# Kernel tuning notes

Hardware: AMD Instinct MI355X
Metric: run time of the kernel (lower is better)

## Reference

```python
import jax, jax.numpy as jnp
import numpy as np

N_WAY, N_SHOT = 10, 15
N_QUERY, D = 8192, 1024
C_REG = 0.1
MAX_ITER = 15


def setup_inputs() -> dict:
    key = jax.random.key(0)
    k1, k2 = jax.random.split(key)
    n_sup = N_WAY * N_SHOT
    feat = jax.random.normal(k1, (n_sup + N_QUERY, D), dtype=jnp.float32) * 0.1
    label_support = jnp.arange(N_WAY, dtype=jnp.int32)
    label_query = jax.random.randint(k2, (N_QUERY,), 0, N_WAY, dtype=jnp.int32)
    scale = jnp.ones((1,), dtype=jnp.float32)
    return {"feat": feat, "label_support": label_support,
            "label_query": label_query, "scale": scale}


def _qp_solve(Q, p, h, A):
    """min 0.5 z'Qz + p'z  s.t.  z <= h,  A z = 0.
    Infeasible-start primal-dual interior-point method, MAX_ITER fixed iterations
    (mirrors qpth's QPFunction(maxIter=15) iterative batched-solve structure)."""
    n = Q.shape[0]
    m = A.shape[0]
    dtype = Q.dtype
    z = h - 1.0                      # slack s = h - z = 1 > 0
    s = jnp.ones((n,), dtype)
    lam = jnp.ones((n,), dtype)
    nu = jnp.zeros((m,), dtype)
    sigma = jnp.asarray(0.1, dtype)  # centering parameter

    def step(carry, _):
        z, s, lam, nu = carry
        mu = jnp.dot(s, lam) / n
        rd = Q @ z + p + lam + A.T @ nu      # dual residual
        rp = A @ z                           # primal (equality) residual, b = 0
        rc = s * lam - sigma * mu            # complementarity residual
        r1 = -rd + rc / s
        H = Q + jnp.diag(lam / s)
        L = jnp.linalg.cholesky(H)
        solveH = lambda r: jax.scipy.linalg.cho_solve((L, True), r)
        Hinv_AT = solveH(A.T)                # (n, m)
        Hinv_r1 = solveH(r1)                 # (n,)
        S = A @ Hinv_AT                      # (m, m) Schur complement
        dnu = jnp.linalg.solve(S, A @ Hinv_r1 + rp)
        dz = Hinv_r1 - Hinv_AT @ dnu
        ds = -dz
        dlam = (lam * dz - rc) / s

        def max_step(v, dv):                 # largest alpha keeping v + alpha*dv > 0
            ratios = jnp.where(dv < 0, -v / jnp.where(dv < 0, dv, -1.0), jnp.inf)
            return jnp.min(ratios)

        alpha = jnp.minimum(1.0, 0.99 * jnp.minimum(max_step(s, ds), max_step(lam, dlam)))
        return (z + alpha * dz, s + alpha * ds, lam + alpha * dlam, nu + alpha * dnu), None

    (z, s, lam, nu), _ = jax.lax.scan(step, (z, s, lam, nu), None, length=MAX_ITER)
    return z


def reference(feat, label_support, label_query, scale):
    n_way, n_shot = N_WAY, N_SHOT
    n_sup = n_way * n_shot
    support = feat[:n_sup]                       # (n_sup, d)
    query = feat[n_sup:]                         # (n_q, d)
    sup_labels = jnp.repeat(label_support, n_shot)   # label[0].repeat_interleave(n_shot)

    K = support @ support.T                      # Gram matrix (n_sup, n_sup)
    n = n_sup * n_way
    eye_w = jnp.eye(n_way, dtype=K.dtype)
    # batched_kronecker(K, I_way): index (i*n_way + a)
    Q = jnp.einsum('ij,ab->iajb', K, eye_w).reshape(n, n) + 10.0 * jnp.eye(n, dtype=K.dtype)
    y_onehot = jax.nn.one_hot(sup_labels, n_way, dtype=K.dtype).reshape(n)
    p = -y_onehot                                # e
    h = C_REG * y_onehot                         # box: z <= C_reg * Y (C = I)
    # A = kron(I_{n_sup}, ones(1, n_way))
    A = jnp.einsum('ij,a->ija', jnp.eye(n_sup, dtype=K.dtype),
                   jnp.ones((n_way,), K.dtype)).reshape(n_sup, n)

    qp_sol = _qp_solve(Q, p, h, A).reshape(n_sup, n_way)

    compat = support @ query.T                   # (n_sup, n_q)
    # logits[q, w] = sum_s compat[s, q] * qp_sol[s, w]
    logits = scale[0] * jnp.einsum('sq,sw->qw', compat, qp_sol)
    log_prb = jax.nn.log_softmax(logits, axis=1)     # (n_q, n_way)
    y_q = jax.nn.one_hot(label_query, n_way, dtype=log_prb.dtype)
    loss = -(y_q * log_prb).sum(axis=1).mean()
    return (log_prb, loss)
```

## Files before the change

kernel.cpp:

```cpp
#include <hip/hip_runtime.h>


#define NW    10
#define NSH   15
#define NSUP  150
#define NQ    8192
#define DIM   1024
#define NVAR  1500
#define NP    152
#define NTT   19
#define NACT  (NTT*NTT)
#define TPB   384
#define SIGMA 0.1f
#define PSTR  68

#define OFF_K     0
#define OFF_Z     22800
#define OFF_S     24300
#define OFF_LAM   25800
#define OFF_R1    27300
#define OFF_DZ    28800
#define OFF_DLAM  30300
#define OFF_G     31800
#define OFF_NU0   33300
#define OFF_NU1   33452
#define OFF_DNU   33604
#define OFF_DOTS  33756
#define OFF_MU    33786
#define OFF_SLOT  33788
#define OFF_LP    33792
#define OFF_WT    35840
#define OFF_SMAT  46080
#define OFF_X     69184
#define XSZ       (NP*NP)

__device__ __forceinline__ void bgj_core(float (&H)[8][8], const int t, const int tr, const int tc,
                                         float (*rowbuf)[PSTR], float (*colbuf)[NTT][PSTR],
                                         float (*wbuf)[PSTR]) {
  const int lane = t & 63;
  const int pr = lane >> 3, pc = lane & 7;
  const int r8 = t & 7;
  const int wj2 = t >> 3;
  const int jb = wj2 >> 1;
  const int jh4 = (wj2 & 1) << 2;
  const bool wact = (t < 8*NTT*2);
  const bool act = (t < NACT);
  for (int kb = 0; kb < NTT; ++kb) {
    const int cur = kb & 1, nxt = cur ^ 1;
    float p = rowbuf[kb][lane];
#pragma unroll
    for (int pp = 0; pp < 8; ++pp) {
      const float pv   = __shfl(p, pp*9, 64);
      const float d    = 1.0f / pv;
      const float rowv = __shfl(p, pp*8 + pc, 64);
      const float colv = __shfl(p, pr*8 + pp, 64);
      const float nr   = rowv * d;
      float v = fmaf(-colv, nr, p);
      if (pr == pp) v = nr;
      if (pc == pp) v = -colv * d;
      if (pr == pp && pc == pp) v = d;
      p = v;
    }
    float pv8[8];
#pragma unroll
    for (int q = 0; q < 8; ++q) pv8[q] = __shfl(p, r8*8 + q, 64);
    if (wact) {
      float w0, w1, w2, w3;
      if (jb == kb) {
        w0 = jh4 ? pv8[4] : pv8[0]; w1 = jh4 ? pv8[5] : pv8[1];
        w2 = jh4 ? pv8[6] : pv8[2]; w3 = jh4 ? pv8[7] : pv8[3];
      } else {
        w0 = w1 = w2 = w3 = 0.0f;
#pragma unroll
        for (int q = 0; q < 8; ++q) {
          const float4 x = *(const float4*)(&rowbuf[jb][q*8 + jh4]);
          w0 = fmaf(pv8[q], x.x, w0); w1 = fmaf(pv8[q], x.y, w1);
          w2 = fmaf(pv8[q], x.z, w2); w3 = fmaf(pv8[q], x.w, w3);
        }
      }
      *(float4*)(&wbuf[jb][r8*8 + jh4]) = make_float4(w0, w1, w2, w3);
    }
    __syncthreads();
    if (act) {
      if (tr == kb) {
        const float4* wsrc = (const float4*)(&wbuf[tc][0]);
#pragma unroll
        for (int r = 0; r < 8; ++r) {
          const float4 x = wsrc[2*r], y = wsrc[2*r+1];
          H[r][0]=x.x; H[r][1]=x.y; H[r][2]=x.z; H[r][3]=x.w;
          H[r][4]=y.x; H[r][5]=y.y; H[r][6]=y.z; H[r][7]=y.w;
        }
      } else {
        float C[8][8];
        const float4* cs = (const float4*)(&colbuf[cur][tr][0]);
#pragma unroll
        for (int r = 0; r < 8; ++r) {
          const float4 x = cs[2*r], y = cs[2*r+1];
          C[r][0]=x.x; C[r][1]=x.y; C[r][2]=x.z; C[r][3]=x.w;
          C[r][4]=y.x; C[r][5]=y.y; C[r][6]=y.z; C[r][7]=y.w;
        }
        if (tc == kb) {
#pragma unroll
          for (int r = 0; r < 8; ++r)
#pragma unroll
            for (int c = 0; c < 8; ++c) H[r][c] = 0.0f;
        }
        const float4* wsrc = (const float4*)(&wbuf[tc][0]);
#pragma unroll
        for (int q = 0; q < 8; ++q) {
          const float4 x = wsrc[2*q], y = wsrc[2*q+1];
          const float w0=x.x,w1=x.y,w2=x.z,w3=x.w,w4=y.x,w5=y.y,w6=y.z,w7=y.w;
#pragma unroll
          for (int r = 0; r < 8; ++r) {
            const float cq = C[r][q];
            H[r][0]=fmaf(-cq,w0,H[r][0]); H[r][1]=fmaf(-cq,w1,H[r][1]);
            H[r][2]=fmaf(-cq,w2,H[r][2]); H[r][3]=fmaf(-cq,w3,H[r][3]);
            H[r][4]=fmaf(-cq,w4,H[r][4]); H[r][5]=fmaf(-cq,w5,H[r][5]);
            H[r][6]=fmaf(-cq,w6,H[r][6]); H[r][7]=fmaf(-cq,w7,H[r][7]);
          }
        }
      }
      if (kb < NTT-1) {
        if (tr == kb+1) {
          float4* dst = (float4*)(&rowbuf[tc][0]);
#pragma unroll
          for (int r = 0; r < 8; ++r) {
            dst[2*r]   = make_float4(H[r][0],H[r][1],H[r][2],H[r][3]);
            dst[2*r+1] = make_float4(H[r][4],H[r][5],H[r][6],H[r][7]);
          }
        }
        if (tc == kb+1) {
          float4* dst = (float4*)(&colbuf[nxt][tr][0]);
#pragma unroll
          for (int r = 0; r < 8; ++r) {
            dst[2*r]   = make_float4(H[r][0],H[r][1],H[r][2],H[r][3]);
            dst[2*r+1] = make_float4(H[r][4],H[r][5],H[r][6],H[r][7]);
          }
        }
      }
    }
    __syncthreads();
  }
}

__global__ __launch_bounds__(256) void k_gram(const float* __restrict__ feat, float* __restrict__ ws) {
  const int bi = blockIdx.x / 10, bj = blockIdx.x % 10;
  const int t = threadIdx.x;
  const int r = t / 15, c = t % 15;
  const bool act = (t < 225);
  __shared__ float As[15][65], Bs[15][65];
  float acc = 0.0f;
  for (int ch = 0; ch < 16; ++ch) {
    for (int idx = t; idx < 960; idx += 256) {
      const int rr = idx >> 6, dd = idx & 63;
      As[rr][dd] = feat[(bi*15+rr)*DIM + ch*64 + dd];
      Bs[rr][dd] = feat[(bj*15+rr)*DIM + ch*64 + dd];
    }
    __syncthreads();
    if (act) {
      for (int dd = 0; dd < 64; ++dd) acc += As[r][dd] * Bs[c][dd];
    }
    __syncthreads();
  }
  if (act) ws[OFF_K + (bi*15+r)*NP + (bj*15+c)] = acc;
}

__global__ __launch_bounds__(TPB, 2) void kqpA(const int* __restrict__ labSup,
                                               float* __restrict__ ws, const int it) {
  const int b = blockIdx.x;
  const int t = threadIdx.x;
  const int tr = t / NTT, tc = t % NTT;
  const bool act = (t < NACT);
  __shared__ __align__(16) float rowbuf[NTT][PSTR], colbuf[2][NTT][PSTR], wbuf[NTT][PSTR];
  __shared__ float zloc[NP], sloc[NP], lloc[NP], dloc[NP], nuloc[NP], r1loc[NP];
  __shared__ float pacc[NP][NTT];
  unsigned* slots = (unsigned*)ws + OFF_SLOT;
  const int p = it & 1;
  float mu;
  if (it == 0) {
    if (t < NSUP) {
      const float y = (labSup[t/NSH] == b) ? 1.0f : 0.0f;
      const float zv = 0.1f*y - 1.0f;
      zloc[t] = zv; sloc[t] = 1.0f; lloc[t] = 1.0f; nuloc[t] = 0.0f;
      const int idx = t*NW + b;
      ws[OFF_Z+idx] = zv; ws[OFF_S+idx] = 1.0f; ws[OFF_LAM+idx] = 1.0f;
      if (b == 0) ws[OFF_NU1 + t] = 0.0f;
    } else if (t < NP) { zloc[t]=0.0f; sloc[t]=0.0f; lloc[t]=0.0f; nuloc[t]=0.0f; }
    mu = 1.0f;
    if (t == 0) slots[p] = 0x7F800000u;
    if (b == 0 && t == 0) ws[OFF_MU] = 1.0f;
  } else {
    const float am = __uint_as_float(slots[p^1]);
    const float alpha = fminf(1.0f, 0.99f * am);
    if (t == 0) slots[p] = 0x7F800000u;
    float D0 = 0.0f, D1 = 0.0f, D2 = 0.0f;
#pragma unroll
    for (int a = 0; a < NW; ++a) {
      D0 += ws[OFF_DOTS + a*3 + 0];
      D1 += ws[OFF_DOTS + a*3 + 1];
      D2 += ws[OFF_DOTS + a*3 + 2];
    }
    mu = (D0 + alpha*D1 - alpha*alpha*D2) / (float)NVAR;
    if (b == 0 && t == 0) ws[OFF_MU] = mu;
    const int nuR = OFF_NU0 + p*NP;
    const int nuW = OFF_NU0 + (p^1)*NP;
    if (t < NSUP) {
      const int idx = t*NW + b;
      const float dzv = ws[OFF_DZ + idx], dlv = ws[OFF_DLAM + idx];
      const float zn = ws[OFF_Z + idx]   + alpha*dzv;
      const float sn = ws[OFF_S + idx]   - alpha*dzv;
      const float ln = ws[OFF_LAM + idx] + alpha*dlv;
      ws[OFF_Z+idx]=zn; ws[OFF_S+idx]=sn; ws[OFF_LAM+idx]=ln;
      zloc[t]=zn; sloc[t]=sn; lloc[t]=ln;
      const float nv = ws[nuR + t] + alpha * ws[OFF_DNU + t];
      nuloc[t] = nv;
      if (b == 0) ws[nuW + t] = nv;
    } else if (t < NP) { zloc[t]=0.0f; sloc[t]=0.0f; lloc[t]=0.0f; nuloc[t]=0.0f; }
  }
  __syncthreads();
  if (t < NSUP) dloc[t] = lloc[t] / sloc[t];
  else if (t < NP) dloc[t] = 0.0f;
  __syncthreads();
  float H[8][8];
  if (act) {
#pragma unroll
    for (int r = 0; r < 8; ++r) {
      const int row = 8*tr + r;
      if (row < NSUP) {
        const float4* ks = (const float4*)(ws + OFF_K + row*NP + 8*tc);
        const float4 x = ks[0], y = ks[1];
        H[r][0]=x.x; H[r][1]=x.y; H[r][2]=x.z; H[r][3]=x.w;
        H[r][4]=y.x; H[r][5]=y.y; H[r][6]=y.z; H[r][7]=y.w;
        if (tc == NTT-1) { H[r][6] = 0.0f; H[r][7] = 0.0f; }
      } else {
#pragma unroll
        for (int c = 0; c < 8; ++c) H[r][c] = 0.0f;
      }
#pragma unroll
      for (int c = 0; c < 8; ++c) {
        const int col = 8*tc + c;
        if (col == row) H[r][c] += (row < NSUP) ? (10.0f + dloc[row]) : 1.0f;
      }
    }
#pragma unroll
    for (int r = 0; r < 8; ++r) {
      float pz = 0.0f;
#pragma unroll
      for (int c = 0; c < 8; ++c) pz = fmaf(H[r][c], zloc[8*tc + c], pz);
      pacc[8*tr + r][tc] = pz;
    }
    if (tr == 0) {
      float4* dst = (float4*)(&rowbuf[tc][0]);
#pragma unroll
      for (int r = 0; r < 8; ++r) {
        dst[2*r]   = make_float4(H[r][0],H[r][1],H[r][2],H[r][3]);
        dst[2*r+1] = make_float4(H[r][4],H[r][5],H[r][6],H[r][7]);
      }
    }
    if (tc == 0) {
      float4* dst = (float4*)(&colbuf[0][tr][0]);
#pragma unroll
      for (int r = 0; r < 8; ++r) {
        dst[2*r]   = make_float4(H[r][0],H[r][1],H[r][2],H[r][3]);
        dst[2*r+1] = make_float4(H[r][4],H[r][5],H[r][6],H[r][7]);
      }
    }
  }
  __syncthreads();
  if (t < NSUP) {
    float hz = 0.0f;
    for (int q = 0; q < NTT; ++q) hz += pacc[t][q];
    const float qz  = hz - dloc[t]*zloc[t];
    const float y   = (labSup[t/NSH] == b) ? 1.0f : 0.0f;
    const float rd  = qz - y + lloc[t] + nuloc[t];
    const float rc  = sloc[t]*lloc[t] - SIGMA*mu;
    const float r1v = -rd + rc/sloc[t];
    ws[OFF_R1 + t*NW + b] = r1v;
    r1loc[t] = r1v;
  } else if (t < NP) r1loc[t] = 0.0f;
  bgj_core(H, t, tr, tc, rowbuf, colbuf, wbuf);
  if (act) {
    float* Xb = ws + OFF_X + b*XSZ;
#pragma unroll
    for (int r = 0; r < 8; ++r) {
      float4* dst = (float4*)(Xb + (8*tr+r)*NP + 8*tc);
      dst[0] = make_float4(H[r][0],H[r][1],H[r][2],H[r][3]);
      dst[1] = make_float4(H[r][4],H[r][5],H[r][6],H[r][7]);
    }
#pragma unroll
    for (int r = 0; r < 8; ++r) {
      float pg = 0.0f;
#pragma unroll
      for (int c = 0; c < 8; ++c) pg = fmaf(H[r][c], r1loc[8*tc+c], pg);
      pacc[8*tr+r][tc] = pg;
    }
  }
  __syncthreads();
  if (t < NSUP) {
    float g = 0.0f;
    for (int q = 0; q < NTT; ++q) g += pacc[t][q];
    ws[OFF_G + t*NW + b] = g;
  }
}

__global__ __launch_bounds__(256) void k_sum(float* __restrict__ ws) {
  for (int idx = blockIdx.x*256 + threadIdx.x; idx < XSZ; idx += gridDim.x*256) {
    float v = 0.0f;
#pragma unroll
    for (int a = 0; a < NW; ++a) v += ws[OFF_X + a*XSZ + idx];
    ws[OFF_SMAT + idx] = v;
  }
}

__global__ __launch_bounds__(TPB, 2) void kqpB(float* __restrict__ ws, const int it) {
  const int b = blockIdx.x;
  const int t = threadIdx.x;
  const int tr = t / NTT, tc = t % NTT;
  const bool act = (t < NACT);
  __shared__ __align__(16) float rowbuf[NTT][PSTR], colbuf[2][NTT][PSTR], wbuf[NTT][PSTR];
  __shared__ float tloc[NP], r1l[NP], vloc[NP];
  __shared__ float pacc[NP][NTT];
  __shared__ float wred[TPB/64][3];
  const float mu = ws[OFF_MU];
  if (t < NP) {
    float v = 0.0f;
    if (t < NSUP) {
      float rp = 0.0f, gs = 0.0f;
#pragma unroll
      for (int a = 0; a < NW; ++a) {
        rp += ws[OFF_Z + t*NW + a];
        gs += ws[OFF_G + t*NW + a];
      }
      v = rp + gs;
      r1l[t] = ws[OFF_R1 + t*NW + b];
    } else r1l[t] = 0.0f;
    tloc[t] = v;
  }
  float Sg[8][8];
  if (act) {
#pragma unroll
    for (int r = 0; r < 8; ++r) {
      const float4* ss = (const float4*)(ws + OFF_SMAT + (8*tr+r)*NP + 8*tc);
      const float4 x = ss[0], y = ss[1];
      Sg[r][0]=x.x; Sg[r][1]=x.y; Sg[r][2]=x.z; Sg[r][3]=x.w;
      Sg[r][4]=y.x; Sg[r][5]=y.y; Sg[r][6]=y.z; Sg[r][7]=y.w;
    }
    if (tr == 0) {
      float4* dst = (float4*)(&rowbuf[tc][0]);
#pragma unroll
      for (int r = 0; r < 8; ++r) {
        dst[2*r]   = make_float4(Sg[r][0],Sg[r][1],Sg[r][2],Sg[r][3]);
        dst[2*r+1] = make_float4(Sg[r][4],Sg[r][5],Sg[r][6],Sg[r][7]);
      }
    }
    if (tc == 0) {
      float4* dst = (float4*)(&colbuf[0][tr][0]);
#pragma unroll
      for (int r = 0; r < 8; ++r) {
        dst[2*r]   = make_float4(Sg[r][0],Sg[r][1],Sg[r][2],Sg[r][3]);
        dst[2*r+1] = make_float4(Sg[r][4],Sg[r][5],Sg[r][6],Sg[r][7]);
      }
    }
  }
  __syncthreads();
  bgj_core(Sg, t, tr, tc, rowbuf, colbuf, wbuf);
  if (act) {
#pragma unroll
    for (int r = 0; r < 8; ++r) {
      float pd = 0.0f;
#pragma unroll
      for (int c = 0; c < 8; ++c) pd = fmaf(Sg[r][c], tloc[8*tc+c], pd);
      pacc[8*tr+r][tc] = pd;
    }
  }
  __syncthreads();
  if (t < NP) {
    float v = 0.0f;
    if (t < NSUP) {
      for (int q = 0; q < NTT; ++q) v += pacc[t][q];
      if (b == 0) ws[OFF_DNU + t] = v;
    }
    vloc[t] = (t < NSUP) ? (r1l[t] - v) : 0.0f;
  }
  __syncthreads();
  if (act) {
    const float* Xb = ws + OFF_X + b*XSZ;
    const int cb = 8*tc;
#pragma unroll
    for (int r = 0; r < 8; ++r) {
      const float4* src = (const float4*)(Xb + (8*tr+r)*NP + cb);
      const float4 v0 = src[0], v1 = src[1];
      pacc[8*tr+r][tc] =
          v0.x*vloc[cb+0] + v0.y*vloc[cb+1] + v0.z*vloc[cb+2] + v0.w*vloc[cb+3]
        + v1.x*vloc[cb+4] + v1.y*vloc[cb+5] + v1.z*vloc[cb+6] + v1.w*vloc[cb+7];
    }
  }
  __syncthreads();
  float d0 = 0.0f, d1 = 0.0f, d2 = 0.0f;
  if (t < NSUP) {
    float dzv = 0.0f;
    for (int q = 0; q < NTT; ++q) dzv += pacc[t][q];
    const int idx = t*NW + b;
    const float svv = ws[OFF_S + idx], lvv = ws[OFF_LAM + idx];
    const float rc  = svv*lvv - SIGMA*mu;
    const float dlv = (lvv*dzv - rc)/svv;
    ws[OFF_DZ + idx]   = dzv;
    ws[OFF_DLAM + idx] = dlv;
    unsigned* slot = (unsigned*)ws + OFF_SLOT + (it & 1);
    const float dsv = -dzv;
    if (dsv < 0.0f) atomicMin(slot, __float_as_uint(-svv/dsv));
    if (dlv < 0.0f) atomicMin(slot, __float_as_uint(-lvv/dlv));
    d0 = svv*lvv;
    d1 = svv*dlv - lvv*dzv;
    d2 = dzv*dlv;
  }
#pragma unroll
  for (int off = 32; off > 0; off >>= 1) {
    d0 += __shfl_xor(d0, off, 64);
    d1 += __shfl_xor(d1, off, 64);
    d2 += __shfl_xor(d2, off, 64);
  }
  if ((t & 63) == 0) { wred[t>>6][0]=d0; wred[t>>6][1]=d1; wred[t>>6][2]=d2; }
  __syncthreads();
  if (t == 0) {
    float s0=0.0f, s1=0.0f, s2=0.0f;
#pragma unroll
    for (int w = 0; w < TPB/64; ++w) { s0+=wred[w][0]; s1+=wred[w][1]; s2+=wred[w][2]; }
    ws[OFF_DOTS + b*3 + 0] = s0;
    ws[OFF_DOTS + b*3 + 1] = s1;
    ws[OFF_DOTS + b*3 + 2] = s2;
  }
}

__global__ __launch_bounds__(1024) void k_wt(const float* __restrict__ feat,
                                             const float* __restrict__ scale,
                                             float* __restrict__ ws) {
  const int w = blockIdx.x;
  const int dd = threadIdx.x;
  __shared__ float zloc[NSUP];
  const float am = __uint_as_float(((unsigned*)ws)[OFF_SLOT + 0]);
  const float alpha = fminf(1.0f, 0.99f * am);
  if (dd < NSUP) {
    const int idx = dd*NW + w;
    zloc[dd] = ws[OFF_Z + idx] + alpha * ws[OFF_DZ + idx];
  }
  __syncthreads();
  float acc = 0.0f;
  for (int ss = 0; ss < NSUP; ++ss)
    acc = fmaf(feat[(size_t)ss*DIM + dd], zloc[ss], acc);
  ws[OFF_WT + w*DIM + dd] = acc * scale[0];
}

__global__ __launch_bounds__(256) void k_logits(const float* __restrict__ feat,
                                                const int* __restrict__ labq,
                                                float* __restrict__ out,
                                                float* __restrict__ ws) {
  const int t = threadIdx.x;
  const int wv = t >> 6, l = t & 63;
  __shared__ float wtl[NW][DIM];
  __shared__ float lpart[4];
  for (int idx = t; idx < NW*DIM; idx += 256) wtl[idx >> 10][idx & 1023] = ws[OFF_WT + idx];
  __syncthreads();
  float lsum = 0.0f;
  const int qbase = blockIdx.x*64 + wv*16;
  for (int i = 0; i < 16; ++i) {
    const int q = qbase + i;
    const float* qrow = feat + (size_t)(NSUP + q)*DIM;
    float acc[NW];
#pragma unroll
    for (int w = 0; w < NW; ++w) acc[w] = 0.0f;
#pragma unroll
    for (int c = 0; c < 4; ++c) {
      const float4 qv = *(const float4*)(qrow + c*256 + 4*l);
#pragma unroll
      for (int w = 0; w < NW; ++w) {
        const float4 wvv = *(const float4*)(&wtl[w][c*256 + 4*l]);
        acc[w] += qv.x*wvv.x + qv.y*wvv.y + qv.z*wvv.z + qv.w*wvv.w;
      }
    }
#pragma unroll
    for (int w = 0; w < NW; ++w) {
#pragma unroll
      for (int off = 32; off > 0; off >>= 1)
        acc[w] += __shfl_xor(acc[w], off, 64);
    }
    float m = acc[0];
#pragma unroll
    for (int w = 1; w < NW; ++w) m = fmaxf(m, acc[w]);
    float se = 0.0f;
#pragma unroll
    for (int w = 0; w < NW; ++w) se += expf(acc[w]-m);
    const float lse = m + logf(se);
    if (l == 0) {
      const int y = labq[q];
      float lpy = 0.0f;
#pragma unroll
      for (int w = 0; w < NW; ++w) {
        const float lp = acc[w] - lse;
        out[q*NW + w] = lp;
        if (w == y) lpy = lp;
      }
      lsum -= lpy;
    }
  }
  if (l == 0) lpart[wv] = lsum;
  __syncthreads();
  if (t == 0) ws[OFF_LP + blockIdx.x] = lpart[0]+lpart[1]+lpart[2]+lpart[3];
}

__global__ __launch_bounds__(128) void k_loss(float* __restrict__ out, const float* __restrict__ ws) {
  const int t = threadIdx.x;
  __shared__ float red[128];
  red[t] = ws[OFF_LP + t];
  __syncthreads();
  for (int off = 64; off > 0; off >>= 1) {
    if (t < off) red[t] += red[t + off];
    __syncthreads();
  }
  if (t == 0) out[NQ*NW] = red[0] / (float)NQ;
}

extern "C" void kernel_launch(void* const* d_in, const int* in_sizes, int n_in,
                              void* d_out, int out_size, void* d_ws, size_t ws_size,
                              hipStream_t stream) {
  const float* feat  = (const float*)d_in[0];
  const int*   labS  = (const int*)d_in[1];
  const int*   labQ  = (const int*)d_in[2];
  const float* scale = (const float*)d_in[3];
  float* ws  = (float*)d_ws;
  float* out = (float*)d_out;

  k_gram<<<100, 256, 0, stream>>>(feat, ws);
  for (int it = 0; it < 15; ++it) {
    kqpA<<<NW, TPB, 0, stream>>>(labS, ws, it);
    k_sum<<<32, 256, 0, stream>>>(ws);
    kqpB<<<NW, TPB, 0, stream>>>(ws, it);
  }
  k_wt<<<NW, 1024, 0, stream>>>(feat, scale, ws);
  k_logits<<<128, 256, 0, stream>>>(feat, labQ, out, ws);
  k_loss<<<1, 128, 0, stream>>>(out, ws);
}
```

Measured before the change: 2.139 ms.

## Pipeline next pivot-block inversion into block Gauss-Jordan loop and vectorize k_sum

The block Gauss-Jordan inversion now computes the next diagonal pivot block ahead of time. Before the first barrier, the owning thread saves its pre-update block to shared memory. After the update phase, every thread rebuilds the updated pivot from the colbuf row and wbuf column and runs the 8x8 shuffle-based inversion, so the serial pivot chain no longer starts each iteration. This trades some redundant FMAs and extra shared-memory reads for a shorter critical path between barriers. The k_sum reduction also switches to float4 loads and stores.

```diff
diff --git a/kernel.cpp b/kernel.cpp
--- a/kernel.cpp
+++ b/kernel.cpp
@@ -34,9 +34,28 @@
 #define OFF_X     69184
 #define XSZ       (NP*NP)
 
+__device__ __forceinline__ void piv_chain(float p, const int pr, const int pc, const int r8,
+                                          float* pv8) {
+#pragma unroll
+  for (int pp = 0; pp < 8; ++pp) {
+    const float pv   = __shfl(p, pp*9, 64);
+    const float d    = 1.0f / pv;
+    const float rowv = __shfl(p, pp*8 + pc, 64);
+    const float colv = __shfl(p, pr*8 + pp, 64);
+    const float nr   = rowv * d;
+    float v = fmaf(-colv, nr, p);
+    if (pr == pp) v = nr;
+    if (pc == pp) v = -colv * d;
+    if (pr == pp && pc == pp) v = d;
+    p = v;
+  }
+#pragma unroll
+  for (int q = 0; q < 8; ++q) pv8[q] = __shfl(p, r8*8 + q, 64);
+}
+
 __device__ __forceinline__ void bgj_core(float (&H)[8][8], const int t, const int tr, const int tc,
                                          float (*rowbuf)[PSTR], float (*colbuf)[NTT][PSTR],
-                                         float (*wbuf)[PSTR]) {
+                                         float (*wbuf)[PSTR], float* pivpre) {
   const int lane = t & 63;
   const int pr = lane >> 3, pc = lane & 7;
   const int r8 = t & 7;
@@ -45,25 +64,10 @@
   const int jh4 = (wj2 & 1) << 2;
   const bool wact = (t < 8*NTT*2);
   const bool act = (t < NACT);
+  float pv8[8];
+  piv_chain(rowbuf[0][lane], pr, pc, r8, pv8);
   for (int kb = 0; kb < NTT; ++kb) {
     const int cur = kb & 1, nxt = cur ^ 1;
-    float p = rowbuf[kb][lane];
-#pragma unroll
-    for (int pp = 0; pp < 8; ++pp) {
-      const float pv   = __shfl(p, pp*9, 64);
-      const float d    = 1.0f / pv;
-      const float rowv = __shfl(p, pp*8 + pc, 64);
-      const float colv = __shfl(p, pr*8 + pp, 64);
-      const float nr   = rowv * d;
-      float v = fmaf(-colv, nr, p);
-      if (pr == pp) v = nr;
-      if (pc == pp) v = -colv * d;
-      if (pr == pp && pc == pp) v = d;
-      p = v;
-    }
-    float pv8[8];
-#pragma unroll
-    for (int q = 0; q < 8; ++q) pv8[q] = __shfl(p, r8*8 + q, 64);
     if (wact) {
       float w0, w1, w2, w3;
       if (jb == kb) {
@@ -80,6 +84,14 @@
       }
       *(float4*)(&wbuf[jb][r8*8 + jh4]) = make_float4(w0, w1, w2, w3);
     }
+    if (act && tr == kb+1 && tc == kb+1) {
+      float4* dst = (float4*)pivpre;
+#pragma unroll
+      for (int r = 0; r < 8; ++r) {
+        dst[2*r]   = make_float4(H[r][0],H[r][1],H[r][2],H[r][3]);
+        dst[2*r+1] = make_float4(H[r][4],H[r][5],H[r][6],H[r][7]);
+      }
+    }
     __syncthreads();
     if (act) {
       if (tr == kb) {
@@ -138,6 +150,15 @@
           }
         }
       }
+    }
+    if (kb < NTT-1) {
+      float pn = pivpre[lane];
+      const float* crow = &colbuf[cur][kb+1][pr*8];
+      const float* wcol = &wbuf[kb+1][pc];
+#pragma unroll
+      for (int q = 0; q < 8; ++q)
+        pn = fmaf(-crow[q], wcol[q*8], pn);
+      piv_chain(pn, pr, pc, r8, pv8);
     }
     __syncthreads();
   }
@@ -172,6 +193,7 @@
   const int tr = t / NTT, tc = t % NTT;
   const bool act = (t < NACT);
   __shared__ __align__(16) float rowbuf[NTT][PSTR], colbuf[2][NTT][PSTR], wbuf[NTT][PSTR];
+  __shared__ __align__(16) float pivpre[64];
   __shared__ float zloc[NP], sloc[NP], lloc[NP], dloc[NP], nuloc[NP], r1loc[NP];
   __shared__ float pacc[NP][NTT];
   unsigned* slots = (unsigned*)ws + OFF_SLOT;
@@ -278,7 +300,7 @@
     ws[OFF_R1 + t*NW + b] = r1v;
     r1loc[t] = r1v;
   } else if (t < NP) r1loc[t] = 0.0f;
-  bgj_core(H, t, tr, tc, rowbuf, colbuf, wbuf);
+  bgj_core(H, t, tr, tc, rowbuf, colbuf, wbuf, pivpre);
   if (act) {
     float* Xb = ws + OFF_X + b*XSZ;
 #pragma unroll
@@ -304,11 +326,15 @@
 }
 
 __global__ __launch_bounds__(256) void k_sum(float* __restrict__ ws) {
-  for (int idx = blockIdx.x*256 + threadIdx.x; idx < XSZ; idx += gridDim.x*256) {
-    float v = 0.0f;
-#pragma unroll
-    for (int a = 0; a < NW; ++a) v += ws[OFF_X + a*XSZ + idx];
-    ws[OFF_SMAT + idx] = v;
+  const int n4 = XSZ/4;
+  for (int idx = blockIdx.x*256 + threadIdx.x; idx < n4; idx += gridDim.x*256) {
+    float4 v = make_float4(0.0f, 0.0f, 0.0f, 0.0f);
+#pragma unroll
+    for (int a = 0; a < NW; ++a) {
+      const float4 x = *(const float4*)(ws + OFF_X + a*XSZ + idx*4);
+      v.x += x.x; v.y += x.y; v.z += x.z; v.w += x.w;
+    }
+    *(float4*)(ws + OFF_SMAT + idx*4) = v;
   }
 }
 
@@ -318,6 +344,7 @@
   const int tr = t / NTT, tc = t % NTT;
   const bool act = (t < NACT);
   __shared__ __align__(16) float rowbuf[NTT][PSTR], colbuf[2][NTT][PSTR], wbuf[NTT][PSTR];
+  __shared__ __align__(16) float pivpre[64];
   __shared__ float tloc[NP], r1l[NP], vloc[NP];
   __shared__ float pacc[NP][NTT];
   __shared__ float wred[TPB/64][3];
@@ -363,7 +390,7 @@
     }
   }
   __syncthreads();
-  bgj_core(Sg, t, tr, tc, rowbuf, colbuf, wbuf);
+  bgj_core(Sg, t, tr, tc, rowbuf, colbuf, wbuf, pivpre);
   if (act) {
 #pragma unroll
     for (int r = 0; r < 8; ++r) {
```

Result: slower. 2.428 ms (+13.5%).
